# Optimization experiments

Hardware: AMD Instinct MI355X
Metric: run time of the kernel (lower is better)

The kernel has to match this reference:

```python
import jax, jax.numpy as jnp
import numpy as np

N = 50000
E = 800000
IN = 128
HEADS = 4
C = 32  # out_features per head
HC = HEADS * C


def setup_inputs() -> dict:
    key = jax.random.key(0)
    ks = jax.random.split(key, 10)
    s_in = 1.0 / np.sqrt(IN)
    x = jax.random.normal(ks[0], (N, IN), dtype=jnp.float32)
    edge_index = jax.random.randint(ks[1], (2, E), 0, N, dtype=jnp.int64)
    Wq = jax.random.normal(ks[2], (IN, HC), dtype=jnp.float32) * s_in
    bq = jnp.zeros((HC,), dtype=jnp.float32)
    Wk = jax.random.normal(ks[3], (IN, HC), dtype=jnp.float32) * s_in
    bk = jnp.zeros((HC,), dtype=jnp.float32)
    Wv = jax.random.normal(ks[4], (IN, HC), dtype=jnp.float32) * s_in
    bv = jnp.zeros((HC,), dtype=jnp.float32)
    Wskip = jax.random.normal(ks[5], (IN, HC), dtype=jnp.float32) * s_in
    bskip = jnp.zeros((HC,), dtype=jnp.float32)
    return {"x": x, "edge_index": edge_index, "Wq": Wq, "bq": bq,
            "Wk": Wk, "bk": bk, "Wv": Wv, "bv": bv,
            "Wskip": Wskip, "bskip": bskip}


def reference(x, edge_index, Wq, bq, Wk, bk, Wv, bv, Wskip, bskip):
    src = edge_index[0]  # message source j
    dst = edge_index[1]  # message target i

    q = (x @ Wq + bq).reshape(N, HEADS, C)
    k = (x @ Wk + bk).reshape(N, HEADS, C)
    v = (x @ Wv + bv).reshape(N, HEADS, C)

    # per-edge attention logits: [E, H]
    logits = jnp.einsum('ehc,ehc->eh', q[dst], k[src]) / jnp.sqrt(
        jnp.asarray(C, dtype=x.dtype))

    # segment softmax over incoming edges of each target node
    seg_max = jax.ops.segment_max(logits, dst, num_segments=N)
    seg_max = jnp.where(jnp.isfinite(seg_max), seg_max, 0.0)
    expd = jnp.exp(logits - seg_max[dst])
    seg_sum = jax.ops.segment_sum(expd, dst, num_segments=N)
    alpha = expd / (seg_sum[dst] + 1e-16)  # [E, H]

    # scatter-add weighted values: [N, H, C]
    msgs = alpha[:, :, None] * v[src]
    out = jax.ops.segment_sum(msgs, dst, num_segments=N)
    out = out.reshape(N, HC) + (x @ Wskip + bskip)  # root/skip connection

    # LeakyReLU(negative_slope=0.2)
    return jnp.where(out >= 0, out, 0.2 * out)
```

## Files before the change

kernel.cpp:

```cpp
#include <hip/hip_runtime.h>

#define N_NODES 50000
#define E_EDGES 800000
#define IN_F 128
#define HC 128
#define ROWTILES 3125
#define PACK_BLOCKS 32
#define GEMM_BLOCKS 1563
#define CAP 64

typedef __attribute__((ext_vector_type(8))) short short8;
typedef __attribute__((ext_vector_type(4))) float floatx4;

__device__ __forceinline__ unsigned short f2bf(float f) {
    union { float f; unsigned u; } x; x.f = f;
    unsigned r = x.u + 0x7FFF + ((x.u >> 16) & 1);
    return (unsigned short)(r >> 16);
}
__device__ __forceinline__ float bflo(unsigned u) {
    union { unsigned u; float f; } c; c.u = u << 16; return c.f;
}
__device__ __forceinline__ float bfhi(unsigned u) {
    union { unsigned u; float f; } c; c.u = u & 0xFFFF0000u; return c.f;
}
__device__ __forceinline__ int swzb(int b) { return b ^ (((b >> 10) & 3) << 5); }
__device__ __forceinline__ int swzf(int b) { return b ^ (((b >> 11) & 3) << 5); }

__global__ __launch_bounds__(256) void pack_w(
    const float* __restrict__ Wq, const float* __restrict__ Wk,
    const float* __restrict__ Wv, const float* __restrict__ Ws,
    const float* __restrict__ bq, const float* __restrict__ bk,
    const float* __restrict__ bv, const float* __restrict__ bs,
    short* __restrict__ bpack, float* __restrict__ bcat,
    int* __restrict__ cnt)
{
    int t = blockIdx.x * 256 + threadIdx.x;
    int lane = t & 63, ks = (t >> 6) & 3, nt = t >> 8;
    int col = nt * 16 + (lane & 15);
    int sec = col >> 7, c = col & 127;
    const float* W = sec == 0 ? Wq : sec == 1 ? Wk : sec == 2 ? Wv : Ws;
    int kbase = ks * 32 + (lane >> 4) * 8;
    short8 b;
#pragma unroll
    for (int j = 0; j < 8; j++) b[j] = (short)f2bf(W[(size_t)(kbase + j) * HC + c]);
    *(short8*)(bpack + (size_t)t * 8) = b;
    if (t < 512) {
        int s2 = t >> 7, c2 = t & 127;
        bcat[t] = (s2 == 0 ? bq : s2 == 1 ? bk : s2 == 2 ? bv : bs)[c2];
    }
    for (int i = t; i < N_NODES; i += PACK_BLOCKS * 256) cnt[i] = 0;
}

__global__ __launch_bounds__(512) void hist_k(
    const int* __restrict__ src, const int* __restrict__ dst,
    int* __restrict__ cnt, int* __restrict__ ssrc)
{
    int e = blockIdx.x * 512 + threadIdx.x;
    if (e < E_EDGES) {
        int d = dst[e];
        int r = atomicAdd(&cnt[d], 1);
        if (r < CAP) ssrc[(size_t)d * CAP + r] = src[e];
    }
}

__global__ __launch_bounds__(256) void gemm_k(
    const float* __restrict__ x, const short* __restrict__ bpack,
    const float* __restrict__ bcat,
    unsigned short* __restrict__ q, unsigned* __restrict__ kv,
    float* __restrict__ out)
{
    __shared__ __align__(16) unsigned char lds[2 * 20480];

    const int cg = threadIdx.x >> 6;
    const int lane = threadIdx.x & 63;
    const int l16 = lane & 15, kh = lane >> 4;
    const int rt0 = blockIdx.x * 2;
    const bool has1 = (rt0 + 1) < ROWTILES;

    short8 a[2][4];
#pragma unroll
    for (int t = 0; t < 2; t++) {
        const size_t row = (size_t)(t && has1 ? rt0 + 1 : rt0) * 16 + l16;
#pragma unroll
        for (int ks = 0; ks < 4; ks++) {
            const float* p0 = x + row * IN_F + ks * 32 + kh * 8;
            float4 lo = *(const float4*)p0;
            float4 hi = *(const float4*)(p0 + 4);
            short8 aa;
            aa[0] = (short)f2bf(lo.x); aa[1] = (short)f2bf(lo.y);
            aa[2] = (short)f2bf(lo.z); aa[3] = (short)f2bf(lo.w);
            aa[4] = (short)f2bf(hi.x); aa[5] = (short)f2bf(hi.y);
            aa[6] = (short)f2bf(hi.z); aa[7] = (short)f2bf(hi.w);
            a[t][ks] = aa;
        }
    }

    float bias[8];
#pragma unroll
    for (int n = 0; n < 8; n++) bias[n] = bcat[cg * 128 + n * 16 + l16];

    unsigned char* E0b = lds + cg * 4096;
    unsigned char* E1b = lds + 20480 + cg * 4096;
    unsigned char* E0f = lds + 12288;
    unsigned char* E1f = lds + 20480 + 12288;

    const int ntb = cg * 8;
    short8 bc[4], bn[4];
#pragma unroll
    for (int ks = 0; ks < 4; ks++)
        bc[ks] = *(const short8*)(bpack + ((size_t)(ntb * 4 + ks) * 64 + lane) * 8);

#pragma unroll 1
    for (int nt8 = 0; nt8 < 8; nt8++) {
        if (nt8 < 7) {
#pragma unroll
            for (int ks = 0; ks < 4; ks++)
                bn[ks] = *(const short8*)(bpack + ((size_t)((ntb + nt8 + 1) * 4 + ks) * 64 + lane) * 8);
        }
        floatx4 acc0 = {0.f, 0.f, 0.f, 0.f}, acc1 = {0.f, 0.f, 0.f, 0.f};
#pragma unroll
        for (int ks = 0; ks < 4; ks++) {
            acc0 = __builtin_amdgcn_mfma_f32_16x16x32_bf16(a[0][ks], bc[ks], acc0, 0, 0, 0);
            acc1 = __builtin_amdgcn_mfma_f32_16x16x32_bf16(a[1][ks], bc[ks], acc1, 0, 0, 0);
        }
        const float bs_ = bias[nt8];
        if (cg < 3) {
#pragma unroll
            for (int r = 0; r < 4; r++) {
                int boff = ((kh * 4 + r) * 128 + nt8 * 16 + l16) * 2;
                *(unsigned short*)(E0b + swzb(boff)) = f2bf(acc0[r] + bs_);
                *(unsigned short*)(E1b + swzb(boff)) = f2bf(acc1[r] + bs_);
            }
        } else {
#pragma unroll
            for (int r = 0; r < 4; r++) {
                int boff = ((kh * 4 + r) * 128 + nt8 * 16 + l16) * 4;
                *(float*)(E0f + swzf(boff)) = acc0[r] + bs_;
                *(float*)(E1f + swzf(boff)) = acc1[r] + bs_;
            }
        }
#pragma unroll
        for (int ks = 0; ks < 4; ks++) bc[ks] = bn[ks];
    }

    if (cg == 0) {
        unsigned short* g0 = q + (size_t)rt0 * 16 * HC;
#pragma unroll
        for (int i = 0; i < 4; i++) {
            int idx = i * 64 + lane;
            *(uint4*)(g0 + idx * 8) = *(const uint4*)(E0b + swzb(idx * 16));
        }
        if (has1) {
            unsigned short* g1 = q + (size_t)(rt0 + 1) * 16 * HC;
#pragma unroll
            for (int i = 0; i < 4; i++) {
                int idx = i * 64 + lane;
                *(uint4*)(g1 + idx * 8) = *(const uint4*)(E1b + swzb(idx * 16));
            }
        }
    } else if (cg == 3) {
        float* g0 = out + (size_t)rt0 * 16 * HC;
#pragma unroll
        for (int i = 0; i < 8; i++) {
            int idx = i * 64 + lane;
            *(float4*)(g0 + idx * 4) = *(const float4*)(E0f + swzf(idx * 16));
        }
        if (has1) {
            float* g1 = out + (size_t)(rt0 + 1) * 16 * HC;
#pragma unroll
            for (int i = 0; i < 8; i++) {
                int idx = i * 64 + lane;
                *(float4*)(g1 + idx * 4) = *(const float4*)(E1f + swzf(idx * 16));
            }
        }
    }

    __syncthreads();

    if (cg == 1 || (cg == 2 && has1)) {
        const int tsel = cg - 1;
        const unsigned char* Ek = lds + tsel * 20480 + 4096;
        const unsigned char* Ev = lds + tsel * 20480 + 8192;
        const int rtg = rt0 + tsel;
        unsigned* gkv = kv + (size_t)rtg * 16 * 64 * 2;
#pragma unroll
        for (int i = 0; i < 8; i++) {
            int u = i * 64 + lane;
            int row = u >> 5;
            int c0 = (u & 31) * 2;
            int boff = row * 256 + c0 * 4;
            uint2 kp = *(const uint2*)(Ek + swzb(boff));
            uint2 vp = *(const uint2*)(Ev + swzb(boff));
            uint4 o; o.x = kp.x; o.y = vp.x; o.z = kp.y; o.w = vp.y;
            *(uint4*)(gkv + ((size_t)row * 64 + c0) * 2) = o;
        }
    }
}

__global__ __launch_bounds__(256) void node_attn(
    const unsigned short* __restrict__ q, const unsigned* __restrict__ kv,
    const int* __restrict__ cnt, const int* __restrict__ ssrc,
    float* __restrict__ out)
{
    const int wave = (blockIdx.x * 256 + threadIdx.x) >> 6;
    if (wave >= N_NODES) return;
    const int lane = threadIdx.x & 63;
    const int node = wave;

    const unsigned uq = *(const unsigned*)(q + (size_t)node * HC + lane * 2);
    const float qx = bflo(uq), qy = bfhi(uq);

    float accx = 0.f, accy = 0.f, ssum = 0.f;
    int deg = __builtin_amdgcn_readfirstlane(cnt[node]);
    if (deg > CAP) deg = CAP;
    const int* sp = ssrc + (size_t)node * CAP;
    const float scale = 0.17677669529663687f;

    for (int e0 = 0; e0 < deg; e0 += 8) {
        int jj[8];
#pragma unroll
        for (int t = 0; t < 8; t++) {
            int ee = e0 + t;
            jj[t] = sp[ee < deg ? ee : 0];
        }
        uint2 kvu[8];
#pragma unroll
        for (int t = 0; t < 8; t++)
            kvu[t] = *(const uint2*)(kv + ((size_t)jj[t] * 64 + lane) * 2);

        float p[8];
#pragma unroll
        for (int t = 0; t < 8; t++)
            p[t] = qx * bflo(kvu[t].x) + qy * bfhi(kvu[t].x);
#pragma unroll
        for (int off = 1; off <= 8; off <<= 1) {
#pragma unroll
            for (int t = 0; t < 8; t++) p[t] += __shfl_xor(p[t], off);
        }
#pragma unroll
        for (int t = 0; t < 8; t++) {
            float wgt = __expf(p[t] * scale);
            wgt = (e0 + t < deg) ? wgt : 0.f;
            ssum += wgt;
            accx += wgt * bflo(kvu[t].y);
            accy += wgt * bfhi(kvu[t].y);
        }
    }

    const float inv = 1.0f / (ssum + 1e-16f);
    const float2 sk = *(const float2*)(out + (size_t)node * HC + lane * 2);
    float ox = accx * inv + sk.x;
    float oy = accy * inv + sk.y;
    ox = ox >= 0.f ? ox : 0.2f * ox;
    oy = oy >= 0.f ? oy : 0.2f * oy;
    *(float2*)(out + (size_t)node * HC + lane * 2) = make_float2(ox, oy);
}

extern "C" void kernel_launch(void* const* d_in, const int* in_sizes, int n_in,
                              void* d_out, int out_size, void* d_ws, size_t ws_size,
                              hipStream_t stream)
{
    const float* x    = (const float*)d_in[0];
    const int*   ei   = (const int*)d_in[1];
    const float* Wq   = (const float*)d_in[2];
    const float* bq   = (const float*)d_in[3];
    const float* Wk   = (const float*)d_in[4];
    const float* bk   = (const float*)d_in[5];
    const float* Wv   = (const float*)d_in[6];
    const float* bv   = (const float*)d_in[7];
    const float* Wsk  = (const float*)d_in[8];
    const float* bsk  = (const float*)d_in[9];
    float* out = (float*)d_out;

    char* w = (char*)d_ws;
    const size_t NFB = (size_t)N_NODES * HC * sizeof(unsigned short);
    unsigned short* q = (unsigned short*)w;            w += NFB;
    unsigned* kv = (unsigned*)w;                       w += (size_t)N_NODES * 512;
    short* bpack = (short*)w;                          w += 8192 * 8 * sizeof(short);
    float* bcat  = (float*)w;                          w += 512 * sizeof(float);
    int* cnt  = (int*)w;                               w += N_NODES * sizeof(int);
    int* ssrc = (int*)w;

    const int* srcIdx = ei;
    const int* dstIdx = ei + E_EDGES;

    pack_w<<<PACK_BLOCKS, 256, 0, stream>>>(Wq, Wk, Wv, Wsk, bq, bk, bv, bsk,
                                            bpack, bcat, cnt);
    hist_k<<<(E_EDGES + 511) / 512, 512, 0, stream>>>(srcIdx, dstIdx, cnt, ssrc);
    gemm_k<<<GEMM_BLOCKS, 256, 0, stream>>>(x, bpack, bcat, q, kv, out);
    node_attn<<<(N_NODES * 64) / 256, 256, 0, stream>>>(q, kv, cnt, ssrc, out);
}
```

Before: 145.6 us.

## Fuse all four stages into one persistent cooperative kernel with grid syncs

Replaces the four separate launches (weight pack, edge histogram, projection GEMM, node attention) with one cooperative persistent kernel. Grid-wide syncs separate the phases, and the histogram fill is placed alongside the GEMM work inside a single phase. The aim is to remove launch gaps and per-kernel tail effects between stages. In exchange it depends on cooperative launch support, adds grid-sync cost, and runs the GEMM and attention with a grid capped by occupancy instead of one block per tile. The old multi-kernel path is kept as a fallback.

```diff
diff --git a/kernel.cpp b/kernel.cpp
--- a/kernel.cpp
+++ b/kernel.cpp
@@ -1,13 +1,17 @@
 #include <hip/hip_runtime.h>
+#include <hip/hip_cooperative_groups.h>
+
+namespace cgx = cooperative_groups;
 
 #define N_NODES 50000
 #define E_EDGES 800000
 #define IN_F 128
 #define HC 128
 #define ROWTILES 3125
+#define VTILES 1563
+#define CAP 64
 #define PACK_BLOCKS 32
 #define GEMM_BLOCKS 1563
-#define CAP 64
 
 typedef __attribute__((ext_vector_type(8))) short short8;
 typedef __attribute__((ext_vector_type(4))) float floatx4;
@@ -25,6 +29,219 @@
 }
 __device__ __forceinline__ int swzb(int b) { return b ^ (((b >> 10) & 3) << 5); }
 __device__ __forceinline__ int swzf(int b) { return b ^ (((b >> 11) & 3) << 5); }
+
+__global__ __launch_bounds__(256, 4) void mega(
+    const float* __restrict__ x,
+    const float* __restrict__ Wq, const float* __restrict__ Wk,
+    const float* __restrict__ Wv, const float* __restrict__ Ws,
+    const float* __restrict__ bq, const float* __restrict__ bk,
+    const float* __restrict__ bv, const float* __restrict__ bs,
+    const int* __restrict__ src, const int* __restrict__ dstI,
+    unsigned short* __restrict__ q, unsigned* __restrict__ kv,
+    float* __restrict__ out,
+    short* __restrict__ bpack, float* __restrict__ bcat,
+    int* __restrict__ cnt, int* __restrict__ ssrc)
+{
+    __shared__ __align__(16) unsigned char lds[2][12288];
+
+    const int tid = threadIdx.x;
+    const int bid = blockIdx.x;
+    const int nblk = gridDim.x;
+    const int lane = tid & 63;
+    const int cg = tid >> 6;
+    const int l16 = lane & 15, kh = lane >> 4;
+
+    for (int i = bid * 256 + tid; i < N_NODES; i += nblk * 256) cnt[i] = 0;
+    if (bid < PACK_BLOCKS) {
+        int t = bid * 256 + tid;
+        int pl = t & 63, ks = (t >> 6) & 3, nt = t >> 8;
+        int col = nt * 16 + (pl & 15);
+        int sec = col >> 7, c = col & 127;
+        const float* W = sec == 0 ? Wq : sec == 1 ? Wk : sec == 2 ? Wv : Ws;
+        int kbase = ks * 32 + (pl >> 4) * 8;
+        short8 b;
+#pragma unroll
+        for (int j = 0; j < 8; j++)
+            b[j] = (short)f2bf(W[(size_t)(kbase + j) * HC + c]);
+        *(short8*)(bpack + (size_t)t * 8) = b;
+        if (t < 512) {
+            int s2 = t >> 7, c2 = t & 127;
+            bcat[t] = (s2 == 0 ? bq : s2 == 1 ? bk : s2 == 2 ? bv : bs)[c2];
+        }
+    }
+    __threadfence();
+    cgx::this_grid().sync();
+
+    for (int e = bid * 256 + tid; e < E_EDGES; e += nblk * 256) {
+        int d = dstI[e];
+        int r = atomicAdd(&cnt[d], 1);
+        if (r < CAP) ssrc[(size_t)d * CAP + r] = src[e];
+    }
+
+    float bias[8];
+#pragma unroll
+    for (int n = 0; n < 8; n++) bias[n] = bcat[cg * 128 + n * 16 + l16];
+
+    for (int vb = bid; vb < VTILES; vb += nblk) {
+        const int rt0 = vb * 2;
+        const bool has1 = (rt0 + 1) < ROWTILES;
+        __syncthreads();
+
+        short8 a[2][4];
+#pragma unroll
+        for (int t = 0; t < 2; t++) {
+            const size_t row = (size_t)(t && has1 ? rt0 + 1 : rt0) * 16 + l16;
+#pragma unroll
+            for (int ks = 0; ks < 4; ks++) {
+                const float* p0 = x + row * IN_F + ks * 32 + kh * 8;
+                float4 lo = *(const float4*)p0;
+                float4 hi = *(const float4*)(p0 + 4);
+                short8 aa;
+                aa[0] = (short)f2bf(lo.x); aa[1] = (short)f2bf(lo.y);
+                aa[2] = (short)f2bf(lo.z); aa[3] = (short)f2bf(lo.w);
+                aa[4] = (short)f2bf(hi.x); aa[5] = (short)f2bf(hi.y);
+                aa[6] = (short)f2bf(hi.z); aa[7] = (short)f2bf(hi.w);
+                a[t][ks] = aa;
+            }
+        }
+
+        unsigned char* E0 = lds[0] + (cg < 3 ? cg * 4096 : 0);
+        unsigned char* E1 = lds[1] + (cg < 3 ? cg * 4096 : 0);
+
+        const int ntb = cg * 8;
+        short8 bc[4], bn[4];
+#pragma unroll
+        for (int ks = 0; ks < 4; ks++)
+            bc[ks] = *(const short8*)(bpack + ((size_t)(ntb * 4 + ks) * 64 + lane) * 8);
+
+#pragma unroll 1
+        for (int nt8 = 0; nt8 < 8; nt8++) {
+            if (nt8 < 7) {
+#pragma unroll
+                for (int ks = 0; ks < 4; ks++)
+                    bn[ks] = *(const short8*)(bpack + ((size_t)((ntb + nt8 + 1) * 4 + ks) * 64 + lane) * 8);
+            }
+            floatx4 acc0 = {0.f, 0.f, 0.f, 0.f}, acc1 = {0.f, 0.f, 0.f, 0.f};
+#pragma unroll
+            for (int ks = 0; ks < 4; ks++) {
+                acc0 = __builtin_amdgcn_mfma_f32_16x16x32_bf16(a[0][ks], bc[ks], acc0, 0, 0, 0);
+                acc1 = __builtin_amdgcn_mfma_f32_16x16x32_bf16(a[1][ks], bc[ks], acc1, 0, 0, 0);
+            }
+            const float bs_ = bias[nt8];
+            if (cg < 3) {
+#pragma unroll
+                for (int r = 0; r < 4; r++) {
+                    int boff = ((kh * 4 + r) * 128 + nt8 * 16 + l16) * 2;
+                    *(unsigned short*)(E0 + swzb(boff)) = f2bf(acc0[r] + bs_);
+                    *(unsigned short*)(E1 + swzb(boff)) = f2bf(acc1[r] + bs_);
+                }
+            } else {
+                const int c = nt8 * 16 + l16;
+#pragma unroll
+                for (int r = 0; r < 4; r++)
+                    out[(size_t)(rt0 * 16 + kh * 4 + r) * HC + c] = acc0[r] + bs_;
+                if (has1) {
+#pragma unroll
+                    for (int r = 0; r < 4; r++)
+                        out[(size_t)((rt0 + 1) * 16 + kh * 4 + r) * HC + c] = acc1[r] + bs_;
+                }
+            }
+#pragma unroll
+            for (int ks = 0; ks < 4; ks++) bc[ks] = bn[ks];
+        }
+
+        if (cg == 0) {
+            unsigned short* g0 = q + (size_t)rt0 * 16 * HC;
+#pragma unroll
+            for (int i = 0; i < 4; i++) {
+                int idx = i * 64 + lane;
+                *(uint4*)(g0 + idx * 8) = *(const uint4*)(E0 + swzb(idx * 16));
+            }
+            if (has1) {
+                unsigned short* g1 = q + (size_t)(rt0 + 1) * 16 * HC;
+#pragma unroll
+                for (int i = 0; i < 4; i++) {
+                    int idx = i * 64 + lane;
+                    *(uint4*)(g1 + idx * 8) = *(const uint4*)(E1 + swzb(idx * 16));
+                }
+            }
+        }
+
+        __syncthreads();
+
+        if (cg == 1 || (cg == 2 && has1)) {
+            const int tsel = cg - 1;
+            const unsigned char* Ek = lds[tsel] + 4096;
+            const unsigned char* Ev = lds[tsel] + 8192;
+            const int rtg = rt0 + tsel;
+            unsigned* gkv = kv + (size_t)rtg * 16 * 64 * 2;
+#pragma unroll
+            for (int i = 0; i < 8; i++) {
+                int u = i * 64 + lane;
+                int row = u >> 5;
+                int c0 = (u & 31) * 2;
+                int boff = row * 256 + c0 * 4;
+                uint2 kp = *(const uint2*)(Ek + swzb(boff));
+                uint2 vp = *(const uint2*)(Ev + swzb(boff));
+                uint4 o; o.x = kp.x; o.y = vp.x; o.z = kp.y; o.w = vp.y;
+                *(uint4*)(gkv + ((size_t)row * 64 + c0) * 2) = o;
+            }
+        }
+    }
+    __threadfence();
+    cgx::this_grid().sync();
+
+    const int gw = (bid * 256 + tid) >> 6;
+    const float scale = 0.17677669529663687f;
+    for (int node = gw; node < N_NODES; node += nblk * 4) {
+        const unsigned uq = *(const unsigned*)(q + (size_t)node * HC + lane * 2);
+        const float qx = bflo(uq), qy = bfhi(uq);
+
+        float accx = 0.f, accy = 0.f, ssum = 0.f;
+        int deg = __builtin_amdgcn_readfirstlane(cnt[node]);
+        if (deg > CAP) deg = CAP;
+        const int* sp = ssrc + (size_t)node * CAP;
+
+        for (int e0 = 0; e0 < deg; e0 += 8) {
+            int jj[8];
+#pragma unroll
+            for (int t = 0; t < 8; t++) {
+                int ee = e0 + t;
+                jj[t] = sp[ee < deg ? ee : 0];
+            }
+            uint2 kvu[8];
+#pragma unroll
+            for (int t = 0; t < 8; t++)
+                kvu[t] = *(const uint2*)(kv + ((size_t)jj[t] * 64 + lane) * 2);
+
+            float p[8];
+#pragma unroll
+            for (int t = 0; t < 8; t++)
+                p[t] = qx * bflo(kvu[t].x) + qy * bfhi(kvu[t].x);
+#pragma unroll
+            for (int off = 1; off <= 8; off <<= 1) {
+#pragma unroll
+                for (int t = 0; t < 8; t++) p[t] += __shfl_xor(p[t], off);
+            }
+#pragma unroll
+            for (int t = 0; t < 8; t++) {
+                float wgt = __expf(p[t] * scale);
+                wgt = (e0 + t < deg) ? wgt : 0.f;
+                ssum += wgt;
+                accx += wgt * bflo(kvu[t].y);
+                accy += wgt * bfhi(kvu[t].y);
+            }
+        }
+
+        const float inv = 1.0f / (ssum + 1e-16f);
+        const float2 sk = *(const float2*)(out + (size_t)node * HC + lane * 2);
+        float ox = accx * inv + sk.x;
+        float oy = accy * inv + sk.y;
+        ox = ox >= 0.f ? ox : 0.2f * ox;
+        oy = oy >= 0.f ? oy : 0.2f * oy;
+        *(float2*)(out + (size_t)node * HC + lane * 2) = make_float2(ox, oy);
+    }
+}
 
 __global__ __launch_bounds__(256) void pack_w(
     const float* __restrict__ Wq, const float* __restrict__ Wk,
@@ -284,9 +501,31 @@
     const int* srcIdx = ei;
     const int* dstIdx = ei + E_EDGES;
 
-    pack_w<<<PACK_BLOCKS, 256, 0, stream>>>(Wq, Wk, Wv, Wsk, bq, bk, bv, bsk,
-                                            bpack, bcat, cnt);
-    hist_k<<<(E_EDGES + 511) / 512, 512, 0, stream>>>(srcIdx, dstIdx, cnt, ssrc);
-    gemm_k<<<GEMM_BLOCKS, 256, 0, stream>>>(x, bpack, bcat, q, kv, out);
-    node_attn<<<(N_NODES * 64) / 256, 256, 0, stream>>>(q, kv, cnt, ssrc, out);
-}
+    int dev = 0;
+    hipGetDevice(&dev);
+    int numCU = 0;
+    hipDeviceGetAttribute(&numCU, hipDeviceAttributeMultiprocessorCount, dev);
+    int maxB = 0;
+    hipOccupancyMaxActiveBlocksPerMultiprocessor(&maxB, (const void*)mega, 256, 0);
+
+    hipError_t err = hipErrorUnknown;
+    if (maxB > 0 && numCU > 0) {
+        int grid = maxB * numCU;
+        if (grid < PACK_BLOCKS) grid = PACK_BLOCKS;
+        void* args[] = { (void*)&x, (void*)&Wq, (void*)&Wk, (void*)&Wv, (void*)&Wsk,
+                         (void*)&bq, (void*)&bk, (void*)&bv, (void*)&bsk,
+                         (void*)&srcIdx, (void*)&dstIdx,
+                         (void*)&q, (void*)&kv, (void*)&out,
+                         (void*)&bpack, (void*)&bcat, (void*)&cnt, (void*)&ssrc };
+        err = hipLaunchCooperativeKernel((const void*)mega, dim3(grid), dim3(256),
+                                         args, 0, stream);
+    }
+    if (err != hipSuccess) {
+        (void)hipGetLastError();
+        pack_w<<<PACK_BLOCKS, 256, 0, stream>>>(Wq, Wk, Wv, Wsk, bq, bk, bv, bsk,
+                                                bpack, bcat, cnt);
+        hist_k<<<(E_EDGES + 511) / 512, 512, 0, stream>>>(srcIdx, dstIdx, cnt, ssrc);
+        gemm_k<<<GEMM_BLOCKS, 256, 0, stream>>>(x, bpack, bcat, q, kv, out);
+        node_attn<<<(N_NODES * 64) / 256, 256, 0, stream>>>(q, kv, cnt, ssrc, out);
+    }
+}
```

Result: slower. 403.4 us (+177.1%).

## Fuse weight packing with edge histogram and write skip output directly

Applied to the files above, without the earlier changes.

Merges the weight-pack and edge-histogram kernels into one launch, with blocks split by index, and moves the count zeroing to a memset. The gemm kernel no longer stages the fp32 skip-connection tile in LDS. Instead it writes accumulators straight to global memory, which cuts LDS from 40KB to 24KB per block and may raise occupancy. In exchange the direct fp32 stores are strided rather than coalesced float4 writes.

```diff
diff --git a/kernel.cpp b/kernel.cpp
--- a/kernel.cpp
+++ b/kernel.cpp
@@ -6,6 +6,7 @@
 #define HC 128
 #define ROWTILES 3125
 #define PACK_BLOCKS 32
+#define HIST_BLOCKS 3125
 #define GEMM_BLOCKS 1563
 #define CAP 64
 
@@ -24,39 +25,33 @@
     union { unsigned u; float f; } c; c.u = u & 0xFFFF0000u; return c.f;
 }
 __device__ __forceinline__ int swzb(int b) { return b ^ (((b >> 10) & 3) << 5); }
-__device__ __forceinline__ int swzf(int b) { return b ^ (((b >> 11) & 3) << 5); }
-
-__global__ __launch_bounds__(256) void pack_w(
+
+__global__ __launch_bounds__(256) void pack_hist_k(
     const float* __restrict__ Wq, const float* __restrict__ Wk,
     const float* __restrict__ Wv, const float* __restrict__ Ws,
     const float* __restrict__ bq, const float* __restrict__ bk,
     const float* __restrict__ bv, const float* __restrict__ bs,
     short* __restrict__ bpack, float* __restrict__ bcat,
-    int* __restrict__ cnt)
-{
-    int t = blockIdx.x * 256 + threadIdx.x;
-    int lane = t & 63, ks = (t >> 6) & 3, nt = t >> 8;
-    int col = nt * 16 + (lane & 15);
-    int sec = col >> 7, c = col & 127;
-    const float* W = sec == 0 ? Wq : sec == 1 ? Wk : sec == 2 ? Wv : Ws;
-    int kbase = ks * 32 + (lane >> 4) * 8;
-    short8 b;
-#pragma unroll
-    for (int j = 0; j < 8; j++) b[j] = (short)f2bf(W[(size_t)(kbase + j) * HC + c]);
-    *(short8*)(bpack + (size_t)t * 8) = b;
-    if (t < 512) {
-        int s2 = t >> 7, c2 = t & 127;
-        bcat[t] = (s2 == 0 ? bq : s2 == 1 ? bk : s2 == 2 ? bv : bs)[c2];
-    }
-    for (int i = t; i < N_NODES; i += PACK_BLOCKS * 256) cnt[i] = 0;
-}
-
-__global__ __launch_bounds__(512) void hist_k(
     const int* __restrict__ src, const int* __restrict__ dst,
     int* __restrict__ cnt, int* __restrict__ ssrc)
 {
-    int e = blockIdx.x * 512 + threadIdx.x;
-    if (e < E_EDGES) {
+    if (blockIdx.x < PACK_BLOCKS) {
+        int t = blockIdx.x * 256 + threadIdx.x;
+        int lane = t & 63, ks = (t >> 6) & 3, nt = t >> 8;
+        int col = nt * 16 + (lane & 15);
+        int sec = col >> 7, c = col & 127;
+        const float* W = sec == 0 ? Wq : sec == 1 ? Wk : sec == 2 ? Wv : Ws;
+        int kbase = ks * 32 + (lane >> 4) * 8;
+        short8 b;
+#pragma unroll
+        for (int j = 0; j < 8; j++) b[j] = (short)f2bf(W[(size_t)(kbase + j) * HC + c]);
+        *(short8*)(bpack + (size_t)t * 8) = b;
+        if (t < 512) {
+            int s2 = t >> 7, c2 = t & 127;
+            bcat[t] = (s2 == 0 ? bq : s2 == 1 ? bk : s2 == 2 ? bv : bs)[c2];
+        }
+    } else {
+        int e = (blockIdx.x - PACK_BLOCKS) * 256 + threadIdx.x;
         int d = dst[e];
         int r = atomicAdd(&cnt[d], 1);
         if (r < CAP) ssrc[(size_t)d * CAP + r] = src[e];
@@ -69,7 +64,7 @@
     unsigned short* __restrict__ q, unsigned* __restrict__ kv,
     float* __restrict__ out)
 {
-    __shared__ __align__(16) unsigned char lds[2 * 20480];
+    __shared__ __align__(16) unsigned char lds[2][12288];
 
     const int cg = threadIdx.x >> 6;
     const int lane = threadIdx.x & 63;
@@ -99,10 +94,8 @@
 #pragma unroll
     for (int n = 0; n < 8; n++) bias[n] = bcat[cg * 128 + n * 16 + l16];
 
-    unsigned char* E0b = lds + cg * 4096;
-    unsigned char* E1b = lds + 20480 + cg * 4096;
-    unsigned char* E0f = lds + 12288;
-    unsigned char* E1f = lds + 20480 + 12288;
+    unsigned char* E0 = lds[0] + (cg < 3 ? cg * 4096 : 0);
+    unsigned char* E1 = lds[1] + (cg < 3 ? cg * 4096 : 0);
 
     const int ntb = cg * 8;
     short8 bc[4], bn[4];
@@ -128,15 +121,18 @@
 #pragma unroll
             for (int r = 0; r < 4; r++) {
                 int boff = ((kh * 4 + r) * 128 + nt8 * 16 + l16) * 2;
-                *(unsigned short*)(E0b + swzb(boff)) = f2bf(acc0[r] + bs_);
-                *(unsigned short*)(E1b + swzb(boff)) = f2bf(acc1[r] + bs_);
+                *(unsigned short*)(E0 + swzb(boff)) = f2bf(acc0[r] + bs_);
+                *(unsigned short*)(E1 + swzb(boff)) = f2bf(acc1[r] + bs_);
             }
         } else {
-#pragma unroll
-            for (int r = 0; r < 4; r++) {
-                int boff = ((kh * 4 + r) * 128 + nt8 * 16 + l16) * 4;
-                *(float*)(E0f + swzf(boff)) = acc0[r] + bs_;
-                *(float*)(E1f + swzf(boff)) = acc1[r] + bs_;
+            const int c = nt8 * 16 + l16;
+#pragma unroll
+            for (int r = 0; r < 4; r++)
+                out[(size_t)(rt0 * 16 + kh * 4 + r) * HC + c] = acc0[r] + bs_;
+            if (has1) {
+#pragma unroll
+                for (int r = 0; r < 4; r++)
+                    out[(size_t)((rt0 + 1) * 16 + kh * 4 + r) * HC + c] = acc1[r] + bs_;
             }
         }
 #pragma unroll
@@ -148,29 +144,14 @@
 #pragma unroll
         for (int i = 0; i < 4; i++) {
             int idx = i * 64 + lane;
-            *(uint4*)(g0 + idx * 8) = *(const uint4*)(E0b + swzb(idx * 16));
+            *(uint4*)(g0 + idx * 8) = *(const uint4*)(E0 + swzb(idx * 16));
         }
         if (has1) {
             unsigned short* g1 = q + (size_t)(rt0 + 1) * 16 * HC;
 #pragma unroll
             for (int i = 0; i < 4; i++) {
                 int idx = i * 64 + lane;
-                *(uint4*)(g1 + idx * 8) = *(const uint4*)(E1b + swzb(idx * 16));
-            }
-        }
-    } else if (cg == 3) {
-        float* g0 = out + (size_t)rt0 * 16 * HC;
-#pragma unroll
-        for (int i = 0; i < 8; i++) {
-            int idx = i * 64 + lane;
-            *(float4*)(g0 + idx * 4) = *(const float4*)(E0f + swzf(idx * 16));
-        }
-        if (has1) {
-            float* g1 = out + (size_t)(rt0 + 1) * 16 * HC;
-#pragma unroll
-            for (int i = 0; i < 8; i++) {
-                int idx = i * 64 + lane;
-                *(float4*)(g1 + idx * 4) = *(const float4*)(E1f + swzf(idx * 16));
+                *(uint4*)(g1 + idx * 8) = *(const uint4*)(E1 + swzb(idx * 16));
             }
         }
     }
@@ -179,8 +160,8 @@
 
     if (cg == 1 || (cg == 2 && has1)) {
         const int tsel = cg - 1;
-        const unsigned char* Ek = lds + tsel * 20480 + 4096;
-        const unsigned char* Ev = lds + tsel * 20480 + 8192;
+        const unsigned char* Ek = lds[tsel] + 4096;
+        const unsigned char* Ev = lds[tsel] + 8192;
         const int rtg = rt0 + tsel;
         unsigned* gkv = kv + (size_t)rtg * 16 * 64 * 2;
 #pragma unroll
@@ -284,9 +265,10 @@
     const int* srcIdx = ei;
     const int* dstIdx = ei + E_EDGES;
 
-    pack_w<<<PACK_BLOCKS, 256, 0, stream>>>(Wq, Wk, Wv, Wsk, bq, bk, bv, bsk,
-                                            bpack, bcat, cnt);
-    hist_k<<<(E_EDGES + 511) / 512, 512, 0, stream>>>(srcIdx, dstIdx, cnt, ssrc);
+    hipMemsetAsync(cnt, 0, N_NODES * sizeof(int), stream);
+    pack_hist_k<<<PACK_BLOCKS + HIST_BLOCKS, 256, 0, stream>>>(
+        Wq, Wk, Wv, Wsk, bq, bk, bv, bsk, bpack, bcat,
+        srcIdx, dstIdx, cnt, ssrc);
     gemm_k<<<GEMM_BLOCKS, 256, 0, stream>>>(x, bpack, bcat, q, kv, out);
     node_attn<<<(N_NODES * 64) / 256, 256, 0, stream>>>(q, kv, cnt, ssrc, out);
 }
```

New measurement: 149.3 us. +2.5%, slower.
